# Kernel tuning notes

Hardware: AMD Instinct MI355X
Metric: run time of the kernel (lower is better)

The kernel has to match this reference:

```python
import jax, jax.numpy as jnp
import numpy as np

BATCH, T, MAXLEN, DMODEL = 8, 32, 8, 256
UNITS = MAXLEN * DMODEL  # 2048, GRU units == input_dim


def setup_inputs() -> dict:
    key = jax.random.key(0)
    k1, k2, k3, k4, k5 = jax.random.split(key, 5)
    scale = 1.0 / np.sqrt(UNITS)
    x = jax.random.normal(k1, (BATCH, T, MAXLEN, DMODEL), jnp.float32)
    h0 = jax.random.normal(k2, (BATCH, UNITS), jnp.float32) * 0.1
    W = jax.random.normal(k3, (UNITS, 3 * UNITS), jnp.float32) * scale  # input kernel
    U = jax.random.normal(k4, (UNITS, 3 * UNITS), jnp.float32) * scale  # recurrent kernel
    b = jax.random.normal(k5, (2, 3 * UNITS), jnp.float32) * 0.01  # [input_bias, recurrent_bias] (reset_after)
    return {"x": x, "h0": h0, "W": W, "U": U, "b": b}


def _gru_seq(xp, h0, U, b_rec):
    """Run GRU (Keras v2, reset_after=True) over precomputed input projections.
    xp: (B, T, 3U) = x @ W + b_in ; h0: (B, U). Returns ((B,T,U) states, (B,U) last)."""
    def step(h, xp_t):
        rec = h @ U + b_rec  # (B, 3U)
        xz, xr, xh = jnp.split(xp_t, 3, axis=-1)
        rz, rr, rh = jnp.split(rec, 3, axis=-1)
        z = jax.nn.sigmoid(xz + rz)
        r = jax.nn.sigmoid(xr + rr)
        hh = jnp.tanh(xh + r * rh)
        h_new = z * h + (1.0 - z) * hh
        return h_new, h_new
    h_last, hs = jax.lax.scan(step, h0, jnp.swapaxes(xp, 0, 1))
    return jnp.swapaxes(hs, 0, 1), h_last


def reference(x, h0, W, U, b):
    # x: (B, T, M, d). Causal branch: for each mask row i, zero out positions > i
    # along the maxLen axis, run the full-sequence GRU, keep slice i of output.
    B, T, M, d = x.shape
    units = M * d
    b_in, b_rec = b[0], b[1]
    masks = jnp.tril(jnp.ones((M, M), x.dtype))  # (M, M) lower triangular
    # Fold the M mask variants into the batch dim -> one fused scan.
    xm = (x[None] * masks[:, None, None, :, None]).reshape(M * B, T, units)
    xp = jnp.einsum('bti,iu->btu', xm, W) + b_in  # precompute input projection
    h0r = jnp.broadcast_to(h0[None], (M, B, units)).reshape(M * B, units)
    hs, h_last = _gru_seq(xp, h0r, U, b_rec)
    out = hs.reshape(M, B, T, M, d)
    idx = jnp.arange(M)
    ret = out[idx, :, :, idx, :]            # (M, B, T, d): slice i of variant i
    ret = jnp.transpose(ret, (1, 2, 0, 3))  # (B, T, M, d)
    state = h_last.reshape(M, B, units)[M - 1]  # state from last (full-mask) run
    return ret, state
```

## Files before the change

### kernel.cpp

```cpp
#include <hip/hip_runtime.h>
#include <hip/hip_bf16.h>

typedef _Float16 f16x8 __attribute__((ext_vector_type(8)));
typedef float f32x4 __attribute__((ext_vector_type(4)));
typedef unsigned long long ull;

#define UNITS   2048
#define NC      6144
#define TSTEPS  32
#define HSTRIDE 131072

__device__ __forceinline__ float sigmoid_f(float v){ return 1.0f/(1.0f+__expf(-v)); }

__global__ __launch_bounds__(256) void prep_misc(
    const float* __restrict__ x, const float* __restrict__ h0,
    _Float16* __restrict__ xh, _Float16* __restrict__ hRing,
    unsigned* __restrict__ bar)
{
  int i = blockIdx.x*256 + threadIdx.x;
  if (i < 640) bar[i] = 0;
  if (i < 524288) xh[i] = (_Float16)x[i];
  if (i < 131072) {
    int s = i >> 11, u = i & 2047;
    float v = h0[((s & 7) << 11) + u];
    hRing[(((u >> 3) << 6) + s)*8 + (u & 7)] = (_Float16)v;
  }
}

__global__ __launch_bounds__(256) void transpose_cast(
    const float* __restrict__ W, const float* __restrict__ U,
    _Float16* __restrict__ Wt, _Float16* __restrict__ Ut)
{
  __shared__ float tile[64][65];
  const float* src = blockIdx.z ? U : W;
  _Float16* dst = blockIdx.z ? Ut : Wt;
  int n0 = blockIdx.x*64, k0 = blockIdx.y*64;
  int lane = threadIdx.x & 63, grp = threadIdx.x >> 6;
  #pragma unroll
  for (int r = grp; r < 64; r += 4)
    tile[r][lane] = src[(size_t)(k0+r)*NC + n0 + lane];
  __syncthreads();
  #pragma unroll
  for (int r = grp; r < 64; r += 4)
    dst[(size_t)(n0+r)*UNITS + k0 + lane] = (_Float16)tile[lane][r];
}

__global__ __launch_bounds__(512) void xp_gemm(
    const _Float16* __restrict__ xh, const _Float16* __restrict__ Wt,
    const float* __restrict__ bin, float* __restrict__ xp)
{
  __shared__ __align__(16) short sB[64*256];
  int n0 = blockIdx.x*64, bt0 = blockIdx.y*128;
  int tid = threadIdx.x;
  int lane = tid & 63, w = tid >> 6;
  int wm = w & 3, wn = w >> 2;
  int nl = lane & 15, kg = lane >> 4;
  f32x4 acc[2][2] = {{{0,0,0,0},{0,0,0,0}},{{0,0,0,0},{0,0,0,0}}};
  for (int l = 0; l < 8; ++l) {
    __syncthreads();
    #pragma unroll
    for (int i = 0; i < 4; ++i) {
      int e = tid + i*512;
      int col = e >> 5, ch = e & 31;
      f16x8 v = *(const f16x8*)(Wt + (size_t)(n0+col)*UNITS + l*256 + ch*8);
      int off = ((col<<9) | (ch<<4)) ^ ((col&7)<<4);
      *(f16x8*)((char*)sB + off) = v;
    }
    __syncthreads();
    #pragma unroll
    for (int kk = 0; kk < 256; kk += 32) {
      f16x8 a[2];
      #pragma unroll
      for (int sub = 0; sub < 2; ++sub) {
        int row = bt0 + wm*32 + sub*16 + nl;
        a[sub] = *(const f16x8*)(xh + ((size_t)row*8 + l)*256 + kg*8 + kk);
      }
      #pragma unroll
      for (int nt = 0; nt < 2; ++nt) {
        int col = wn*32 + nt*16 + nl;
        int off = ((col<<9) | ((kk + kg*8)<<1)) ^ ((col&7)<<4);
        f16x8 bfr = *(const f16x8*)((const char*)sB + off);
        #pragma unroll
        for (int sub = 0; sub < 2; ++sub)
          acc[sub][nt] = __builtin_amdgcn_mfma_f32_16x16x32_f16(a[sub], bfr, acc[sub][nt], 0,0,0);
      }
    }
    #pragma unroll
    for (int sub = 0; sub < 2; ++sub) {
      int orow = bt0 + wm*32 + sub*16 + kg*4;
      #pragma unroll
      for (int nt = 0; nt < 2; ++nt) {
        int col = n0 + wn*32 + nt*16 + nl;
        float bv = bin[col];
        #pragma unroll
        for (int r = 0; r < 4; ++r) {
          int rr = orow + r;
          int b_ = rr >> 5, t_ = rr & 31;
          xp[(size_t)((l*8 + b_)*32 + t_)*NC + col] = acc[sub][nt][r] + bv;
        }
      }
    }
  }
}

__device__ __forceinline__ void half_barrier(unsigned* bar, int half, int idxInHalf, int t)
{
  __syncthreads();
  if (threadIdx.x == 0) {
    unsigned* grp  = bar + (half*8 + (idxInHalf & 7))*32;
    unsigned* root = bar + (16 + half)*32;
    unsigned* gen  = bar + (18 + half)*32;
    unsigned tgt = (unsigned)(t + 1);
    unsigned a = __hip_atomic_fetch_add(grp, 1u, __ATOMIC_RELAXED, __HIP_MEMORY_SCOPE_AGENT) + 1u;
    if (a == tgt*16u) {
      unsigned r = __hip_atomic_fetch_add(root, 1u, __ATOMIC_RELAXED, __HIP_MEMORY_SCOPE_AGENT) + 1u;
      if (r == tgt*8u)
        __hip_atomic_store(gen, tgt, __ATOMIC_RELEASE, __HIP_MEMORY_SCOPE_AGENT);
    }
    while (__hip_atomic_load(gen, __ATOMIC_RELAXED, __HIP_MEMORY_SCOPE_AGENT) < tgt)
      __builtin_amdgcn_s_sleep(1);
  }
  __syncthreads();
  __builtin_amdgcn_fence(__ATOMIC_ACQUIRE, "workgroup");
}

__global__ __launch_bounds__(512, 1) void gru_persist(
    const _Float16* __restrict__ Ut, const float* __restrict__ xp, const float* __restrict__ brec,
    const float* __restrict__ h0, _Float16* __restrict__ hRing,
    float* __restrict__ ret, float* __restrict__ st, unsigned* __restrict__ bar)
{
  __shared__ __align__(16) short sU[2*16*2048];
  __shared__ __align__(16) float sRed[6*3*288];
  __shared__ __align__(16) float sGate[2*3*288];

  int tid = threadIdx.x;
  int lane = tid & 63, w = tid >> 6;
  int m = w & 1, kq = w >> 1;
  int half = blockIdx.x & 1;
  int idxInHalf = blockIdx.x >> 1;
  int u0 = idxInHalf * 16;
  int s0 = half * 32;
  int nl = lane & 15, kg = lane >> 4;
  int redidx = lane*4 + (lane>>3)*4;

  #pragma unroll
  for (int i = 0; i < 16; ++i) {
    int e = tid + i*512;
    int g = e >> 12, col = (e >> 8) & 15, ch = e & 255;
    f16x8 v = *(const f16x8*)(Ut + (size_t)(g*UNITS + u0 + col)*UNITS + ch*8);
    int off = ((g<<16) | (col<<12) | (ch<<4)) ^ ((col&7)<<4);
    *(f16x8*)((char*)sU + off) = v;
  }
  f16x8 uh[16];
  #pragma unroll
  for (int kk = 0; kk < 16; ++kk)
    uh[kk] = *(const f16x8*)(Ut + (size_t)(2*UNITS + u0 + nl)*UNITS + kq*512 + kk*32 + kg*8);
  __syncthreads();

  int s_ = tid >> 2, uoff = (tid & 3) * 4;
  int sg = s0 + s_;
  int u4 = u0 + uoff;
  int mp = s_ >> 4, rr_ = s_ & 15, kgp = rr_ >> 2, rp = rr_ & 3;
  int mm = u0 >> 8;

  f32x4 bz4, br4, bh4, hprev;
  if (tid < 128) {
    bz4 = *(const f32x4*)(brec + u4);
    br4 = *(const f32x4*)(brec + 2048 + u4);
    bh4 = *(const f32x4*)(brec + 4096 + u4);
    hprev = *(const f32x4*)(h0 + ((sg & 7) << 11) + u4);
  }

  for (int t = 0; t < TSTEPS; ++t) {
    const _Float16* hc = hRing + (size_t)t*HSTRIDE;
    _Float16*       hn = hRing + (size_t)(t+1)*HSTRIDE;

    f32x4 az = {0,0,0,0}, ar = {0,0,0,0}, ah = {0,0,0,0};
    const _Float16* Ab = hc + (size_t)(((kq*64 + kg)*64) + s0 + m*16 + nl)*8;
    #pragma unroll
    for (int kk = 0; kk < 16; ++kk) {
      f16x8 av = *(const f16x8*)(Ab + kk*2048);
      int kb = (kq*512 + kk*32 + kg*8) << 1;
      int offz = ((0<<16) | (nl<<12) | kb) ^ ((nl&7)<<4);
      int offr = ((1<<16) | (nl<<12) | kb) ^ ((nl&7)<<4);
      f16x8 bz = *(const f16x8*)((const char*)sU + offz);
      f16x8 br = *(const f16x8*)((const char*)sU + offr);
      az = __builtin_amdgcn_mfma_f32_16x16x32_f16(av, bz, az, 0,0,0);
      ar = __builtin_amdgcn_mfma_f32_16x16x32_f16(av, br, ar, 0,0,0);
      ah = __builtin_amdgcn_mfma_f32_16x16x32_f16(av, uh[kk], ah, 0,0,0);
    }

    f32x4 xz4, xr4, xh4;
    if (tid < 128) {
      const float* xrow = xp + ((size_t)sg*32 + t)*NC;
      xz4 = *(const f32x4*)(xrow + u4);
      xr4 = *(const f32x4*)(xrow + 2048 + u4);
      xh4 = *(const f32x4*)(xrow + 4096 + u4);
    }

    if (kq) {
      float* rp_ = &sRed[((kq-1)*2 + m)*3*288 + redidx];
      *(f32x4*)(rp_)       = az;
      *(f32x4*)(rp_ + 288) = ar;
      *(f32x4*)(rp_ + 576) = ah;
    }
    __syncthreads();
    if (kq == 0) {
      #pragma unroll
      for (int p = 0; p < 3; ++p) {
        const float* rp_ = &sRed[(p*2 + m)*3*288 + redidx];
        az += *(const f32x4*)(rp_);
        ar += *(const f32x4*)(rp_ + 288);
        ah += *(const f32x4*)(rp_ + 576);
      }
      float* gp = &sGate[m*3*288 + redidx];
      *(f32x4*)(gp)       = az;
      *(f32x4*)(gp + 288) = ar;
      *(f32x4*)(gp + 576) = ah;
    }
    __syncthreads();

    if (tid < 128) {
      float hv[4];
      ull hw = 0;
      #pragma unroll
      for (int j = 0; j < 4; ++j) {
        int lanep = kgp*16 + uoff + j;
        int gi = mp*3*288 + lanep*4 + (lanep>>3)*4 + rp;
        float vz = sGate[gi];
        float vr = sGate[gi + 288];
        float vh = sGate[gi + 576];
        float z  = sigmoid_f(xz4[j] + vz + bz4[j]);
        float rg = sigmoid_f(xr4[j] + vr + br4[j]);
        float hh = tanhf(xh4[j] + rg*(vh + bh4[j]));
        float hnv = z*hprev[j] + (1.0f - z)*hh;
        hprev[j] = hnv;
        hv[j] = hnv;
        _Float16 hb = (_Float16)hnv;
        hw |= (ull)__builtin_bit_cast(unsigned short, hb) << (16*j);
      }
      __hip_atomic_store((ull*)(hn + (size_t)(((u4 >> 3) << 6) + sg)*8 + (u4 & 7)), hw,
                         __ATOMIC_RELAXED, __HIP_MEMORY_SCOPE_AGENT);
      if ((sg >> 3) == mm) {
        f32x4 o = {hv[0], hv[1], hv[2], hv[3]};
        *(f32x4*)(ret + (size_t)((((sg & 7)*32 + t) << 3) + mm)*256 + (u4 & 255)) = o;
      }
      if (t == 31 && sg >= 56) {
        f32x4 o = {hv[0], hv[1], hv[2], hv[3]};
        *(f32x4*)(st + (size_t)(sg - 56)*UNITS + u4) = o;
      }
    }
    if (t < TSTEPS - 1)
      half_barrier(bar, half, idxInHalf, t);
  }
}

extern "C" void kernel_launch(void* const* d_in, const int* in_sizes, int n_in,
                              void* d_out, int out_size, void* d_ws, size_t ws_size,
                              hipStream_t stream) {
  const float* x  = (const float*)d_in[0];
  const float* h0 = (const float*)d_in[1];
  const float* W  = (const float*)d_in[2];
  const float* U  = (const float*)d_in[3];
  const float* b  = (const float*)d_in[4];
  float* ret = (float*)d_out;
  float* st  = ret + 524288;

  char* p = (char*)d_ws;
  _Float16* Ut = (_Float16*)p; p += 25165824;
  _Float16* Wt = (_Float16*)p; p += 25165824;
  _Float16* xh = (_Float16*)p; p += 1048576;
  float*    xp = (float*)p;    p += 50331648;
  _Float16* hRing = (_Float16*)p; p += 33ull * HSTRIDE * 2;
  unsigned* bar = (unsigned*)p; p += 2560;

  prep_misc<<<2048, 256, 0, stream>>>(x, h0, xh, hRing, bar);
  transpose_cast<<<dim3(96,32,2), 256, 0, stream>>>(W, U, Wt, Ut);
  xp_gemm<<<dim3(96,2), 512, 0, stream>>>(xh, Wt, b, xp);

  const float* brec = b + NC;
  void* args[] = { (void*)&Ut, (void*)&xp, (void*)&brec, (void*)&h0,
                   (void*)&hRing, (void*)&ret, (void*)&st, (void*)&bar };
  hipLaunchCooperativeKernel((const void*)gru_persist, dim3(256), dim3(512),
                             args, 0, stream);
}
```

Baseline: 278.0 us.

## Keep recurrent weights in registers, store input projections as fp16, enlarge GEMM tile

The persistent GRU kernel no longer stages the z/r slices of U in shared memory. Each of 8 waves now holds its 256-wide K-slice of all three gate weights in registers and computes both 16-row state halves, with a wider 8-way shared-memory reduction. The input-projection GEMM covers all 256 rows per block (grid 96) and writes xp as fp16, halving its write and per-step read traffic. Risks are heavy register pressure from 24 f16x8 weight fragments, a larger reduction, and lower precision on the input projections.

```diff
diff --git a/kernel.cpp b/kernel.cpp
--- a/kernel.cpp
+++ b/kernel.cpp
@@ -2,6 +2,7 @@
 #include <hip/hip_bf16.h>
 
 typedef _Float16 f16x8 __attribute__((ext_vector_type(8)));
+typedef _Float16 f16x4 __attribute__((ext_vector_type(4)));
 typedef float f32x4 __attribute__((ext_vector_type(4)));
 typedef unsigned long long ull;
 
@@ -47,15 +48,20 @@
 
 __global__ __launch_bounds__(512) void xp_gemm(
     const _Float16* __restrict__ xh, const _Float16* __restrict__ Wt,
-    const float* __restrict__ bin, float* __restrict__ xp)
+    const float* __restrict__ bin, _Float16* __restrict__ xpf)
 {
   __shared__ __align__(16) short sB[64*256];
-  int n0 = blockIdx.x*64, bt0 = blockIdx.y*128;
+  int n0 = blockIdx.x*64;
   int tid = threadIdx.x;
   int lane = tid & 63, w = tid >> 6;
   int wm = w & 3, wn = w >> 2;
   int nl = lane & 15, kg = lane >> 4;
-  f32x4 acc[2][2] = {{{0,0,0,0},{0,0,0,0}},{{0,0,0,0},{0,0,0,0}}};
+  f32x4 acc[4][2];
+  #pragma unroll
+  for (int sub = 0; sub < 4; ++sub)
+    #pragma unroll
+    for (int nt = 0; nt < 2; ++nt) acc[sub][nt] = (f32x4){0,0,0,0};
+
   for (int l = 0; l < 8; ++l) {
     __syncthreads();
     #pragma unroll
@@ -69,10 +75,10 @@
     __syncthreads();
     #pragma unroll
     for (int kk = 0; kk < 256; kk += 32) {
-      f16x8 a[2];
-      #pragma unroll
-      for (int sub = 0; sub < 2; ++sub) {
-        int row = bt0 + wm*32 + sub*16 + nl;
+      f16x8 a[4];
+      #pragma unroll
+      for (int sub = 0; sub < 4; ++sub) {
+        int row = wm*64 + sub*16 + nl;
         a[sub] = *(const f16x8*)(xh + ((size_t)row*8 + l)*256 + kg*8 + kk);
       }
       #pragma unroll
@@ -81,13 +87,13 @@
         int off = ((col<<9) | ((kk + kg*8)<<1)) ^ ((col&7)<<4);
         f16x8 bfr = *(const f16x8*)((const char*)sB + off);
         #pragma unroll
-        for (int sub = 0; sub < 2; ++sub)
+        for (int sub = 0; sub < 4; ++sub)
           acc[sub][nt] = __builtin_amdgcn_mfma_f32_16x16x32_f16(a[sub], bfr, acc[sub][nt], 0,0,0);
       }
     }
     #pragma unroll
-    for (int sub = 0; sub < 2; ++sub) {
-      int orow = bt0 + wm*32 + sub*16 + kg*4;
+    for (int sub = 0; sub < 4; ++sub) {
+      int orow = wm*64 + sub*16 + kg*4;
       #pragma unroll
       for (int nt = 0; nt < 2; ++nt) {
         int col = n0 + wn*32 + nt*16 + nl;
@@ -96,7 +102,7 @@
         for (int r = 0; r < 4; ++r) {
           int rr = orow + r;
           int b_ = rr >> 5, t_ = rr & 31;
-          xp[(size_t)((l*8 + b_)*32 + t_)*NC + col] = acc[sub][nt][r] + bv;
+          xpf[(size_t)((l*8 + b_)*32 + t_)*NC + col] = (_Float16)(acc[sub][nt][r] + bv);
         }
       }
     }
@@ -124,18 +130,17 @@
   __builtin_amdgcn_fence(__ATOMIC_ACQUIRE, "workgroup");
 }
 
-__global__ __launch_bounds__(512, 1) void gru_persist(
-    const _Float16* __restrict__ Ut, const float* __restrict__ xp, const float* __restrict__ brec,
-    const float* __restrict__ h0, _Float16* __restrict__ hRing,
+__global__ __launch_bounds__(512, 2) void gru_persist(
+    const _Float16* __restrict__ Ut, const _Float16* __restrict__ xpf,
+    const float* __restrict__ brec, const float* __restrict__ h0,
+    _Float16* __restrict__ hRing,
     float* __restrict__ ret, float* __restrict__ st, unsigned* __restrict__ bar)
 {
-  __shared__ __align__(16) short sU[2*16*2048];
-  __shared__ __align__(16) float sRed[6*3*288];
+  __shared__ __align__(16) float sRed[14*3*288];
   __shared__ __align__(16) float sGate[2*3*288];
 
   int tid = threadIdx.x;
-  int lane = tid & 63, w = tid >> 6;
-  int m = w & 1, kq = w >> 1;
+  int lane = tid & 63, kq = tid >> 6;
   int half = blockIdx.x & 1;
   int idxInHalf = blockIdx.x >> 1;
   int u0 = idxInHalf * 16;
@@ -143,19 +148,12 @@
   int nl = lane & 15, kg = lane >> 4;
   int redidx = lane*4 + (lane>>3)*4;
 
-  #pragma unroll
-  for (int i = 0; i < 16; ++i) {
-    int e = tid + i*512;
-    int g = e >> 12, col = (e >> 8) & 15, ch = e & 255;
-    f16x8 v = *(const f16x8*)(Ut + (size_t)(g*UNITS + u0 + col)*UNITS + ch*8);
-    int off = ((g<<16) | (col<<12) | (ch<<4)) ^ ((col&7)<<4);
-    *(f16x8*)((char*)sU + off) = v;
-  }
-  f16x8 uh[16];
-  #pragma unroll
-  for (int kk = 0; kk < 16; ++kk)
-    uh[kk] = *(const f16x8*)(Ut + (size_t)(2*UNITS + u0 + nl)*UNITS + kq*512 + kk*32 + kg*8);
-  __syncthreads();
+  f16x8 uw[3][8];
+  #pragma unroll
+  for (int g = 0; g < 3; ++g)
+    #pragma unroll
+    for (int kk = 0; kk < 8; ++kk)
+      uw[g][kk] = *(const f16x8*)(Ut + (size_t)(g*UNITS + u0 + nl)*UNITS + kq*256 + kk*32 + kg*8);
 
   int s_ = tid >> 2, uoff = (tid & 3) * 4;
   int sg = s0 + s_;
@@ -175,48 +173,60 @@
     const _Float16* hc = hRing + (size_t)t*HSTRIDE;
     _Float16*       hn = hRing + (size_t)(t+1)*HSTRIDE;
 
-    f32x4 az = {0,0,0,0}, ar = {0,0,0,0}, ah = {0,0,0,0};
-    const _Float16* Ab = hc + (size_t)(((kq*64 + kg)*64) + s0 + m*16 + nl)*8;
-    #pragma unroll
-    for (int kk = 0; kk < 16; ++kk) {
-      f16x8 av = *(const f16x8*)(Ab + kk*2048);
-      int kb = (kq*512 + kk*32 + kg*8) << 1;
-      int offz = ((0<<16) | (nl<<12) | kb) ^ ((nl&7)<<4);
-      int offr = ((1<<16) | (nl<<12) | kb) ^ ((nl&7)<<4);
-      f16x8 bz = *(const f16x8*)((const char*)sU + offz);
-      f16x8 br = *(const f16x8*)((const char*)sU + offr);
-      az = __builtin_amdgcn_mfma_f32_16x16x32_f16(av, bz, az, 0,0,0);
-      ar = __builtin_amdgcn_mfma_f32_16x16x32_f16(av, br, ar, 0,0,0);
-      ah = __builtin_amdgcn_mfma_f32_16x16x32_f16(av, uh[kk], ah, 0,0,0);
-    }
-
-    f32x4 xz4, xr4, xh4;
+    f32x4 a0z={0,0,0,0}, a0r={0,0,0,0}, a0h={0,0,0,0};
+    f32x4 a1z={0,0,0,0}, a1r={0,0,0,0}, a1h={0,0,0,0};
+    const _Float16* Ab = hc + (size_t)(((kq*32 + kg)*64) + s0 + nl)*8;
+    #pragma unroll
+    for (int kk = 0; kk < 8; ++kk) {
+      f16x8 av0 = *(const f16x8*)(Ab + kk*2048);
+      f16x8 av1 = *(const f16x8*)(Ab + kk*2048 + 128);
+      a0z = __builtin_amdgcn_mfma_f32_16x16x32_f16(av0, uw[0][kk], a0z, 0,0,0);
+      a1z = __builtin_amdgcn_mfma_f32_16x16x32_f16(av1, uw[0][kk], a1z, 0,0,0);
+      a0r = __builtin_amdgcn_mfma_f32_16x16x32_f16(av0, uw[1][kk], a0r, 0,0,0);
+      a1r = __builtin_amdgcn_mfma_f32_16x16x32_f16(av1, uw[1][kk], a1r, 0,0,0);
+      a0h = __builtin_amdgcn_mfma_f32_16x16x32_f16(av0, uw[2][kk], a0h, 0,0,0);
+      a1h = __builtin_amdgcn_mfma_f32_16x16x32_f16(av1, uw[2][kk], a1h, 0,0,0);
+    }
+
+    f16x4 xz4h, xr4h, xh4h;
     if (tid < 128) {
-      const float* xrow = xp + ((size_t)sg*32 + t)*NC;
-      xz4 = *(const f32x4*)(xrow + u4);
-      xr4 = *(const f32x4*)(xrow + 2048 + u4);
-      xh4 = *(const f32x4*)(xrow + 4096 + u4);
+      const _Float16* xrow = xpf + ((size_t)sg*32 + t)*NC;
+      xz4h = *(const f16x4*)(xrow + u4);
+      xr4h = *(const f16x4*)(xrow + 2048 + u4);
+      xh4h = *(const f16x4*)(xrow + 4096 + u4);
     }
 
     if (kq) {
-      float* rp_ = &sRed[((kq-1)*2 + m)*3*288 + redidx];
-      *(f32x4*)(rp_)       = az;
-      *(f32x4*)(rp_ + 288) = ar;
-      *(f32x4*)(rp_ + 576) = ah;
+      float* rp0 = &sRed[(((kq-1)*2 + 0)*3)*288 + redidx];
+      *(f32x4*)(rp0)        = a0z;
+      *(f32x4*)(rp0 + 288)  = a0r;
+      *(f32x4*)(rp0 + 576)  = a0h;
+      float* rp1 = &sRed[(((kq-1)*2 + 1)*3)*288 + redidx];
+      *(f32x4*)(rp1)        = a1z;
+      *(f32x4*)(rp1 + 288)  = a1r;
+      *(f32x4*)(rp1 + 576)  = a1h;
     }
     __syncthreads();
     if (kq == 0) {
       #pragma unroll
-      for (int p = 0; p < 3; ++p) {
-        const float* rp_ = &sRed[(p*2 + m)*3*288 + redidx];
-        az += *(const f32x4*)(rp_);
-        ar += *(const f32x4*)(rp_ + 288);
-        ah += *(const f32x4*)(rp_ + 576);
-      }
-      float* gp = &sGate[m*3*288 + redidx];
-      *(f32x4*)(gp)       = az;
-      *(f32x4*)(gp + 288) = ar;
-      *(f32x4*)(gp + 576) = ah;
+      for (int p = 0; p < 7; ++p) {
+        const float* q0 = &sRed[((p*2 + 0)*3)*288 + redidx];
+        a0z += *(const f32x4*)(q0);
+        a0r += *(const f32x4*)(q0 + 288);
+        a0h += *(const f32x4*)(q0 + 576);
+        const float* q1 = &sRed[((p*2 + 1)*3)*288 + redidx];
+        a1z += *(const f32x4*)(q1);
+        a1r += *(const f32x4*)(q1 + 288);
+        a1h += *(const f32x4*)(q1 + 576);
+      }
+      float* g0 = &sGate[0*3*288 + redidx];
+      *(f32x4*)(g0)       = a0z;
+      *(f32x4*)(g0 + 288) = a0r;
+      *(f32x4*)(g0 + 576) = a0h;
+      float* g1 = &sGate[1*3*288 + redidx];
+      *(f32x4*)(g1)       = a1z;
+      *(f32x4*)(g1 + 288) = a1r;
+      *(f32x4*)(g1 + 576) = a1h;
     }
     __syncthreads();
 
@@ -230,9 +240,9 @@
         float vz = sGate[gi];
         float vr = sGate[gi + 288];
         float vh = sGate[gi + 576];
-        float z  = sigmoid_f(xz4[j] + vz + bz4[j]);
-        float rg = sigmoid_f(xr4[j] + vr + br4[j]);
-        float hh = tanhf(xh4[j] + rg*(vh + bh4[j]));
+        float z  = sigmoid_f((float)xz4h[j] + vz + bz4[j]);
+        float rg = sigmoid_f((float)xr4h[j] + vr + br4[j]);
+        float hh = tanhf((float)xh4h[j] + rg*(vh + bh4[j]));
         float hnv = z*hprev[j] + (1.0f - z)*hh;
         hprev[j] = hnv;
         hv[j] = hnv;
@@ -270,16 +280,16 @@
   _Float16* Ut = (_Float16*)p; p += 25165824;
   _Float16* Wt = (_Float16*)p; p += 25165824;
   _Float16* xh = (_Float16*)p; p += 1048576;
-  float*    xp = (float*)p;    p += 50331648;
+  _Float16* xpf = (_Float16*)p; p += 25165824;
   _Float16* hRing = (_Float16*)p; p += 33ull * HSTRIDE * 2;
   unsigned* bar = (unsigned*)p; p += 2560;
 
   prep_misc<<<2048, 256, 0, stream>>>(x, h0, xh, hRing, bar);
   transpose_cast<<<dim3(96,32,2), 256, 0, stream>>>(W, U, Wt, Ut);
-  xp_gemm<<<dim3(96,2), 512, 0, stream>>>(xh, Wt, b, xp);
+  xp_gemm<<<96, 512, 0, stream>>>(xh, Wt, b, xpf);
 
   const float* brec = b + NC;
-  void* args[] = { (void*)&Ut, (void*)&xp, (void*)&brec, (void*)&h0,
+  void* args[] = { (void*)&Ut, (void*)&xpf, (void*)&brec, (void*)&h0,
                    (void*)&hRing, (void*)&ret, (void*)&st, (void*)&bar };
   hipLaunchCooperativeKernel((const void*)gru_persist, dim3(256), dim3(512),
                              args, 0, stream);
```

After: 321.0 us. +15.5%, slower.
